# Optimization experiments

Hardware: AMD Instinct MI355X
Metric: run time of the kernel (lower is better)

The kernel has to match this reference:

```python
import jax, jax.numpy as jnp
import numpy as np

DIM = 64        # feature channels of x
HEADS = 4
POS_DIM = 3
NUM_IDS = 8
STR_IN = 512    # strength_linear input size
B, S, W = 4, 1024, 8   # batch, sequence (S1), source-views (S2)


def setup_inputs() -> dict:
    key = jax.random.key(0)
    ks = jax.random.split(key, 18)
    stdv = 1.0 / np.sqrt(DIM * DIM)  # embedding init per module
    d8 = DIM // 8
    u = lambda k, shp, s: jax.random.uniform(k, shp, jnp.float32, -s, s)
    return {
        "x": jax.random.normal(ks[0], (B, DIM, S, W), jnp.float32),
        "pos": jax.random.normal(ks[1], (B, S, POS_DIM), jnp.float32),
        "strength": jax.random.normal(ks[2], (STR_IN,), jnp.float32),
        "embed_id1": 3,
        "q_emb_w": u(ks[3], (NUM_IDS, DIM * DIM), stdv),
        "k_emb_w": u(ks[4], (NUM_IDS, DIM * DIM), stdv),
        "v_emb_w": u(ks[5], (NUM_IDS, DIM * DIM), stdv),
        "pos_w1": u(ks[6], (POS_DIM, POS_DIM), 1.0 / np.sqrt(POS_DIM)),
        "pos_b1": u(ks[7], (POS_DIM,), 1.0 / np.sqrt(POS_DIM)),
        "pos_w2": u(ks[8], (d8, POS_DIM), 1.0 / np.sqrt(POS_DIM)),
        "pos_b2": u(ks[9], (d8,), 1.0 / np.sqrt(POS_DIM)),
        "head_w": u(ks[10], (HEADS, d8), 1.0 / np.sqrt(d8)),
        "head_b": u(ks[11], (HEADS,), 1.0 / np.sqrt(d8)),
        "gate": jnp.ones((HEADS,), jnp.float32),
        "out_w": u(ks[12], (DIM, DIM), 1.0 / np.sqrt(DIM)),
        "out_b": u(ks[13], (DIM,), 1.0 / np.sqrt(DIM)),
        "str_w": u(ks[14], (DIM, STR_IN), 1.0 / np.sqrt(STR_IN)),
        "str_b": u(ks[15], (DIM,), 1.0 / np.sqrt(STR_IN)),
    }


def reference(x, pos, strength, embed_id1, q_emb_w, k_emb_w, v_emb_w,
              pos_w1, pos_b1, pos_w2, pos_b2, head_w, head_b, gate,
              out_w, out_b, str_w, str_b):
    # strength projection: Linear(512, dim)
    s = strength @ str_w.T + str_b                    # [dim]
    xt = jnp.transpose(x, (0, 2, 3, 1))               # [B, S, W, dim]
    qe = q_emb_w[embed_id1].reshape(DIM, DIM)
    ke = k_emb_w[embed_id1].reshape(DIM, DIM)
    ve = v_emb_w[embed_id1].reshape(DIM, DIM)

    def proj(emb):
        y = xt @ emb.T + s                            # [B, S, W, dim]
        # collapse (W, dim) -> (heads, head_dim), heads to axis 1
        y = y.reshape(B, S, HEADS, -1)
        return jnp.transpose(y, (0, 2, 1, 3))         # [B, H, S, hd]

    q, k, v = proj(qe), proj(ke), proj(ve)
    hd = q.shape[-1]
    attn = jax.nn.softmax(jnp.einsum("bhsd,bhtd->bhst", q, k) / np.sqrt(hd), axis=-1)

    # relative-position attention branch
    ph = jax.nn.relu(pos @ pos_w1.T + pos_b1) @ pos_w2.T + pos_b2   # [B, S, dim//8]
    diff = ph[:, :, None, :] - ph[:, None, :, :]                    # [B, S, S, dim//8]
    pos_attn = jnp.transpose(diff @ head_w.T + head_b, (0, 3, 1, 2))
    pos_attn = jax.nn.softmax(pos_attn, axis=-1)                    # [B, H, S, S]

    g = jax.nn.sigmoid(gate).reshape(1, -1, 1, 1)
    attn = (1.0 - g) * attn + g * pos_attn
    attn = attn / jnp.sum(attn, axis=-1, keepdims=True)

    out = jnp.einsum("bhst,bhtd->bhsd", attn, v)      # [B, H, S, hd]
    out = jnp.transpose(out, (0, 2, 1, 3)).reshape(B, S, W, DIM)
    return out @ out_w.T + out_b                      # [B, S, W, dim]
```

## Files before the change

### kernel.cpp

```cpp
#include <hip/hip_runtime.h>
#include <math.h>
#include <stdint.h>

#define B_ 4
#define S_ 1024
#define F_ 512
#define HD 128
#define SOFT_C 4.0f

typedef __attribute__((ext_vector_type(8))) short short8;
typedef __attribute__((ext_vector_type(4))) float f32x4;
typedef __attribute__((ext_vector_type(4))) unsigned int u32x4;
typedef __attribute__((ext_vector_type(2))) unsigned int u32x2;

__device__ __forceinline__ unsigned short f2bf(float f) {
    unsigned int u = __float_as_uint(f);
    u = (u + 0x7FFFu + ((u >> 16) & 1u)) >> 16;
    return (unsigned short)u;
}
__device__ __forceinline__ float bf2f(unsigned int s) {
    return __uint_as_float(s << 16);
}
__device__ __forceinline__ void pack_hilo(const float* v, u32x4& hi, u32x4& lo) {
    #pragma unroll
    for (int p = 0; p < 4; ++p) {
        unsigned int h0 = f2bf(v[2 * p]), h1 = f2bf(v[2 * p + 1]);
        float l0 = v[2 * p] - bf2f(h0), l1 = v[2 * p + 1] - bf2f(h1);
        hi[p] = h0 | (h1 << 16);
        lo[p] = (unsigned int)f2bf(l0) | ((unsigned int)f2bf(l1) << 16);
    }
}

__global__ __launch_bounds__(256) void k_prep(
    const int* __restrict__ embed_id,
    const float* __restrict__ qw, const float* __restrict__ kw,
    const float* __restrict__ vw, const float* __restrict__ ow,
    const float* __restrict__ pos,
    const float* __restrict__ pw1, const float* __restrict__ pb1,
    const float* __restrict__ pw2, const float* __restrict__ pb2,
    const float* __restrict__ head_w,
    const float* __restrict__ strength, const float* __restrict__ str_w,
    const float* __restrict__ str_b,
    unsigned short* __restrict__ packs,
    float* __restrict__ sv, float* __restrict__ svq,
    float* __restrict__ p_g)
{
    __shared__ float red_s[4][4];
    __shared__ float inv_s[4];
    const int blk = blockIdx.x, tid = threadIdx.x;
    const float SCALE = 0.08838834764831845f;

    if (blk < 4) {
        const int id = embed_id[0];
        const float* src = (blk == 0 ? qw + id * 4096 : blk == 1 ? kw + id * 4096
                            : blk == 2 ? vw + id * 4096 : ow);
        const float scale = (blk == 0) ? SCALE : 1.0f;
        unsigned short* hi = packs + blk * 8192;
        unsigned short* lo = hi + 4096;
        for (int i = tid; i < 4096; i += 256) {
            float v = src[i] * scale;
            unsigned short h = f2bf(v);
            hi[i] = h;
            lo[i] = f2bf(v - bf2f(h));
        }
    } else if (blk < 8) {
        const int b = blk - 4;
        const int wv = tid >> 6;
        float w1_[9], b1_[3], w2_[24], b2_[8], hw_[32];
        #pragma unroll
        for (int i = 0; i < 9; ++i)  w1_[i] = pw1[i];
        #pragma unroll
        for (int i = 0; i < 3; ++i)  b1_[i] = pb1[i];
        #pragma unroll
        for (int i = 0; i < 24; ++i) w2_[i] = pw2[i];
        #pragma unroll
        for (int i = 0; i < 8; ++i)  b2_[i] = pb2[i];
        #pragma unroll
        for (int i = 0; i < 32; ++i) hw_[i] = head_w[i];

        float ev[4][4];
        float ps[4] = {0.f, 0.f, 0.f, 0.f};
        #pragma unroll
        for (int k = 0; k < 4; ++k) {
            const int t = k * 256 + tid;
            float p0 = pos[(b * S_ + t) * 3 + 0];
            float p1 = pos[(b * S_ + t) * 3 + 1];
            float p2 = pos[(b * S_ + t) * 3 + 2];
            float h0 = fmaxf(0.f, p0 * w1_[0] + p1 * w1_[1] + p2 * w1_[2] + b1_[0]);
            float h1 = fmaxf(0.f, p0 * w1_[3] + p1 * w1_[4] + p2 * w1_[5] + b1_[1]);
            float h2 = fmaxf(0.f, p0 * w1_[6] + p1 * w1_[7] + p2 * w1_[8] + b1_[2]);
            float ph[8];
            #pragma unroll
            for (int o8 = 0; o8 < 8; ++o8)
                ph[o8] = h0 * w2_[o8 * 3] + h1 * w2_[o8 * 3 + 1] + h2 * w2_[o8 * 3 + 2] + b2_[o8];
            #pragma unroll
            for (int h = 0; h < 4; ++h) {
                float A = 0.f;
                #pragma unroll
                for (int o8 = 0; o8 < 8; ++o8) A += ph[o8] * hw_[h * 8 + o8];
                ev[k][h] = __expf(-A - 1.0f);
                ps[h] += ev[k][h];
            }
        }
        #pragma unroll
        for (int h = 0; h < 4; ++h)
            #pragma unroll
            for (int off = 1; off < 64; off <<= 1)
                ps[h] += __shfl_xor(ps[h], off);
        if ((tid & 63) == 0)
            #pragma unroll
            for (int h = 0; h < 4; ++h) red_s[wv][h] = ps[h];
        __syncthreads();
        if (tid < 4)
            inv_s[tid] = 1.f / (red_s[0][tid] + red_s[1][tid] + red_s[2][tid] + red_s[3][tid]);
        __syncthreads();
        #pragma unroll
        for (int k = 0; k < 4; ++k)
            #pragma unroll
            for (int h = 0; h < 4; ++h)
                p_g[(b * 4 + h) * S_ + k * 256 + tid] = ev[k][h] * inv_s[h];
    } else {
        __shared__ float part_s[4][64];
        const int c = tid & 63, pr = tid >> 6;
        const float* wrow = str_w + c * 512 + pr * 128;
        const float* st   = strength + pr * 128;
        float acc = 0.f;
        #pragma unroll
        for (int j4 = 0; j4 < 32; ++j4) {
            f32x4 wv4 = *(const f32x4*)(wrow + j4 * 4);
            f32x4 s4  = *(const f32x4*)(st + j4 * 4);
            acc += wv4[0] * s4[0] + wv4[1] * s4[1] + wv4[2] * s4[2] + wv4[3] * s4[3];
        }
        part_s[pr][c] = acc;
        __syncthreads();
        if (tid < 64) {
            float v = part_s[0][tid] + part_s[1][tid] + part_s[2][tid]
                    + part_s[3][tid] + str_b[tid];
            sv[tid] = v;
            svq[tid] = v * SCALE;
        }
    }
}

__global__ __launch_bounds__(256) void k_qkv(
    const float* __restrict__ x,
    const unsigned short* __restrict__ packs,
    const float* __restrict__ sv, const float* __restrict__ svq,
    const float* __restrict__ p_g,
    unsigned short* __restrict__ yqh, unsigned short* __restrict__ ykh,
    unsigned short* __restrict__ yvt2, float* __restrict__ xbar)
{
    __shared__ float xr_s[4][8];
    const int tid  = threadIdx.x;
    const int wv   = tid >> 6;
    const int lane = tid & 63;
    const int quad = lane >> 4;
    const int l15  = lane & 15;

    if (blockIdx.x >= 512) {
        const int bi = blockIdx.x - 512;
        const int b = bi >> 6, c = bi & 63;
        const float* xc = x + (size_t)b * 524288 + c * 8192;
        const float* pb = p_g + b * 4096;
        float acc[8] = {};
        #pragma unroll
        for (int rr = 0; rr < 4; ++rr) {
            const int s = tid * 4 + rr;
            f32x4 x0 = *(const f32x4*)(xc + s * 8);
            f32x4 x1 = *(const f32x4*)(xc + s * 8 + 4);
            float p0 = pb[s], p1 = pb[1024 + s], p2 = pb[2048 + s], p3 = pb[3072 + s];
            acc[0] += p0 * x0[0]; acc[1] += p0 * x0[1];
            acc[2] += p1 * x0[2]; acc[3] += p1 * x0[3];
            acc[4] += p2 * x1[0]; acc[5] += p2 * x1[1];
            acc[6] += p3 * x1[2]; acc[7] += p3 * x1[3];
        }
        #pragma unroll
        for (int j = 0; j < 8; ++j)
            #pragma unroll
            for (int off = 1; off < 64; off <<= 1)
                acc[j] += __shfl_xor(acc[j], off);
        if (lane == 0)
            #pragma unroll
            for (int j = 0; j < 8; ++j) xr_s[wv][j] = acc[j];
        __syncthreads();
        if (tid < 8)
            xbar[(b * 8 + tid) * 64 + c] = xr_s[0][tid] + xr_s[1][tid]
                                         + xr_s[2][tid] + xr_s[3][tid];
        return;
    }

    const int r0   = blockIdx.x * 64 + wv * 16;
    const int b    = r0 >> 13;
    const int rloc = (r0 & 8191) + l15;
    const float* xb = x + (size_t)b * 524288;

    u32x4 xhi[2], xlo[2];
    #pragma unroll
    for (int kc = 0; kc < 2; ++kc) {
        float xv[8];
        #pragma unroll
        for (int j = 0; j < 8; ++j)
            xv[j] = xb[(kc * 32 + quad * 8 + j) * 8192 + rloc];
        pack_hilo(xv, xhi[kc], xlo[kc]);
    }

    float svq_l[4], sv_l[4];
    #pragma unroll
    for (int nt = 0; nt < 4; ++nt) {
        svq_l[nt] = svq[nt * 16 + l15];
        sv_l[nt]  = sv[nt * 16 + l15];
    }
    f32x4 svA[4];
    #pragma unroll
    for (int mt = 0; mt < 4; ++mt)
        svA[mt] = *(const f32x4*)(sv + mt * 16 + quad * 4);

    int idxq[4];
    #pragma unroll
    for (int rr = 0; rr < 4; ++rr) {
        const int rl = quad * 4 + rr;
        const int w_ = rl & 7;
        const int s_loc = ((r0 & 8191) >> 3) + (rl >> 3);
        idxq[rr] = (b * 4 + (w_ >> 1)) * 131072 + s_loc * 128 + (w_ & 1) * 64 + l15;
    }

    const int row_g = r0 + l15;
    const int s_idx = (row_g >> 3) & 1023;
    const int w_idx = row_g & 7;
    const int bh    = b * 4 + (w_idx >> 1);
    const int dbase = (w_idx & 1) * 64;
    unsigned short* vtb = yvt2 + (size_t)bh * 131072 + (s_idx >> 6) * 8192
                        + (size_t)dbase * 64 + (s_idx & 63);

    #pragma unroll
    for (int mat = 0; mat < 2; ++mat) {
        const unsigned short* mh = packs + mat * 8192;
        const unsigned short* ml = mh + 4096;
        f32x4 acc[4] = {};
        #pragma unroll
        for (int kc = 0; kc < 2; ++kc)
            #pragma unroll
            for (int nt = 0; nt < 4; ++nt) {
                const int off = (nt * 16 + l15) * 64 + kc * 32 + quad * 8;
                u32x4 ehi = *(const u32x4*)(mh + off);
                u32x4 elo = *(const u32x4*)(ml + off);
                acc[nt] = __builtin_amdgcn_mfma_f32_16x16x32_bf16(
                    __builtin_bit_cast(short8, xhi[kc]),
                    __builtin_bit_cast(short8, ehi), acc[nt], 0, 0, 0);
                acc[nt] = __builtin_amdgcn_mfma_f32_16x16x32_bf16(
                    __builtin_bit_cast(short8, xlo[kc]),
                    __builtin_bit_cast(short8, ehi), acc[nt], 0, 0, 0);
                acc[nt] = __builtin_amdgcn_mfma_f32_16x16x32_bf16(
                    __builtin_bit_cast(short8, xhi[kc]),
                    __builtin_bit_cast(short8, elo), acc[nt], 0, 0, 0);
            }
        unsigned short* y = (mat == 0 ? yqh : ykh);
        const float* svp = (mat == 0 ? svq_l : sv_l);
        #pragma unroll
        for (int nt = 0; nt < 4; ++nt)
            #pragma unroll
            for (int rr = 0; rr < 4; ++rr)
                y[(size_t)idxq[rr] + nt * 16] = f2bf(acc[nt][rr] + svp[nt]);
    }

    {
        const unsigned short* mh = packs + 2 * 8192;
        const unsigned short* ml = mh + 4096;
        f32x4 acc[4] = {};
        #pragma unroll
        for (int kc = 0; kc < 2; ++kc)
            #pragma unroll
            for (int mt = 0; mt < 4; ++mt) {
                const int off = (mt * 16 + l15) * 64 + kc * 32 + quad * 8;
                u32x4 ehi = *(const u32x4*)(mh + off);
                u32x4 elo = *(const u32x4*)(ml + off);
                acc[mt] = __builtin_amdgcn_mfma_f32_16x16x32_bf16(
                    __builtin_bit_cast(short8, ehi),
                    __builtin_bit_cast(short8, xhi[kc]), acc[mt], 0, 0, 0);
                acc[mt] = __builtin_amdgcn_mfma_f32_16x16x32_bf16(
                    __builtin_bit_cast(short8, ehi),
                    __builtin_bit_cast(short8, xlo[kc]), acc[mt], 0, 0, 0);
                acc[mt] = __builtin_amdgcn_mfma_f32_16x16x32_bf16(
                    __builtin_bit_cast(short8, elo),
                    __builtin_bit_cast(short8, xhi[kc]), acc[mt], 0, 0, 0);
            }
        #pragma unroll
        for (int mt = 0; mt < 4; ++mt)
            #pragma unroll
            for (int rr = 0; rr < 4; ++rr) {
                const int c = mt * 16 + quad * 4 + rr;
                vtb[(size_t)c * 64] = f2bf(acc[mt][rr] + svA[mt][rr]);
            }
    }
}

__global__ __launch_bounds__(256, 2) void k_attn(
    const unsigned short* __restrict__ yqh, const unsigned short* __restrict__ ykh,
    const unsigned short* __restrict__ yvt2,
    const float* __restrict__ xbar, const float* __restrict__ vw,
    const int* __restrict__ embed_id, const float* __restrict__ sv,
    const float* __restrict__ gate, float* __restrict__ out)
{
    __shared__ __align__(16) unsigned short kx[2][64 * 136];
    __shared__ __align__(16) unsigned short vx[2][128 * 72];
    __shared__ float vbar_s[128];

    const int tid  = threadIdx.x;
    const int w    = tid >> 6;
    const int lane = tid & 63;
    const int quad = lane >> 4;
    const int l15  = lane & 15;
    const int bh = blockIdx.x & 15, qt = blockIdx.x >> 4;
    const int b = bh >> 2, h = bh & 3;
    const int s0 = qt * 32;
    const int qh = w >> 1;
    const int dh = w & 1;

    const unsigned short* ykb = ykh + (size_t)bh * 131072;
    const unsigned short* yvb = yvt2 + (size_t)bh * 131072;

    if (tid < 128) {
        const int c = tid & 63, wloc = tid >> 6;
        const float* ver = vw + embed_id[0] * 4096 + c * 64;
        const float* xbr = xbar + (b * 8 + h * 2 + wloc) * 64;
        float a = sv[c];
        #pragma unroll
        for (int j4 = 0; j4 < 16; ++j4) {
            f32x4 e4 = *(const f32x4*)(ver + j4 * 4);
            f32x4 x4 = *(const f32x4*)(xbr + j4 * 4);
            a += e4[0] * x4[0] + e4[1] * x4[1] + e4[2] * x4[2] + e4[3] * x4[3];
        }
        vbar_s[wloc * 64 + c] = a;
    }

    u32x4 qf[4];
    #pragma unroll
    for (int kc = 0; kc < 4; ++kc)
        qf[kc] = *(const u32x4*)(yqh + (size_t)bh * 131072
                 + (s0 + qh * 16 + l15) * 128 + kc * 32 + quad * 8);

    #pragma unroll
    for (int r = 0; r < 4; ++r) {
        const int off = r * 2048 + tid * 8;
        *(u32x4*)&kx[0][(off >> 7) * 136 + (off & 127)] =
            *(const u32x4*)(ykb + off);
        *(u32x4*)&vx[0][(off >> 6) * 72 + (off & 63)] =
            *(const u32x4*)(yvb + off);
    }
    __syncthreads();

    f32x4 o[4] = {};
    float lsum = 0.f;
    const int srcA = ((quad & 1) << 5) + l15;

    for (int it = 0; it < 16; ++it) {
        const int cur = it & 1;
        u32x4 kst[4], vst[4];
        const bool pre = (it < 15);
        if (pre) {
            const unsigned short* ksrc = ykb + (it + 1) * 8192;
            const unsigned short* vsrc = yvb + (it + 1) * 8192;
            #pragma unroll
            for (int r = 0; r < 4; ++r)
                kst[r] = *(const u32x4*)(ksrc + r * 2048 + tid * 8);
            #pragma unroll
            for (int r = 0; r < 4; ++r)
                vst[r] = *(const u32x4*)(vsrc + r * 2048 + tid * 8);
        }

        const unsigned short* kxc = kx[cur];
        const unsigned short* vxc = vx[cur];

        #pragma unroll
        for (int th = 0; th < 2; ++th) {
            f32x4 sa0 = {}, sa1 = {};
            #pragma unroll
            for (int kc = 0; kc < 4; ++kc) {
                u32x4 a0 = *(const u32x4*)&kxc[(th * 32 + l15) * 136 + kc * 32 + quad * 8];
                sa0 = __builtin_amdgcn_mfma_f32_16x16x32_bf16(
                    __builtin_bit_cast(short8, a0),
                    __builtin_bit_cast(short8, qf[kc]), sa0, 0, 0, 0);
            }
            #pragma unroll
            for (int kc = 0; kc < 4; ++kc) {
                u32x4 a1 = *(const u32x4*)&kxc[(th * 32 + 16 + l15) * 136 + kc * 32 + quad * 8];
                sa1 = __builtin_amdgcn_mfma_f32_16x16x32_bf16(
                    __builtin_bit_cast(short8, a1),
                    __builtin_bit_cast(short8, qf[kc]), sa1, 0, 0, 0);
            }

            float p0[4], p1[4];
            #pragma unroll
            for (int r = 0; r < 4; ++r) {
                p0[r] = __expf(sa0[r] - SOFT_C);
                p1[r] = __expf(sa1[r] - SOFT_C);
                lsum += p0[r] + p1[r];
            }

            unsigned int pk00 = (unsigned int)f2bf(p0[0]) | ((unsigned int)f2bf(p0[1]) << 16);
            unsigned int pk01 = (unsigned int)f2bf(p0[2]) | ((unsigned int)f2bf(p0[3]) << 16);
            unsigned int pk10 = (unsigned int)f2bf(p1[0]) | ((unsigned int)f2bf(p1[1]) << 16);
            unsigned int pk11 = (unsigned int)f2bf(p1[2]) | ((unsigned int)f2bf(p1[3]) << 16);
            unsigned int sel0 = (quad < 2) ? pk00 : pk10;
            unsigned int sel1 = (quad < 2) ? pk01 : pk11;
            u32x4 pf;
            pf[0] = (unsigned int)__shfl((int)sel0, srcA);
            pf[1] = (unsigned int)__shfl((int)sel1, srcA);
            pf[2] = (unsigned int)__shfl((int)sel0, srcA + 16);
            pf[3] = (unsigned int)__shfl((int)sel1, srcA + 16);

            #pragma unroll
            for (int dt = 0; dt < 4; ++dt) {
                u32x4 vf = *(const u32x4*)&vxc[(dh * 64 + dt * 16 + l15) * 72
                                               + th * 32 + quad * 8];
                o[dt] = __builtin_amdgcn_mfma_f32_16x16x32_bf16(
                    __builtin_bit_cast(short8, vf),
                    __builtin_bit_cast(short8, pf), o[dt], 0, 0, 0);
            }
        }

        if (pre) {
            #pragma unroll
            for (int r = 0; r < 4; ++r) {
                const int off = r * 2048 + tid * 8;
                *(u32x4*)&kx[cur ^ 1][(off >> 7) * 136 + (off & 127)] = kst[r];
            }
            #pragma unroll
            for (int r = 0; r < 4; ++r) {
                const int off = r * 2048 + tid * 8;
                *(u32x4*)&vx[cur ^ 1][(off >> 6) * 72 + (off & 63)] = vst[r];
            }
        }
        __syncthreads();
    }

    lsum += __shfl_xor(lsum, 16);
    lsum += __shfl_xor(lsum, 32);
    const float gf = 1.f / (1.f + __expf(-gate[h]));
    const float cf = (1.f - gf) / lsum;
    const int row = b * S_ + s0 + qh * 16 + l15;
    #pragma unroll
    for (int dt = 0; dt < 4; ++dt) {
        const int d0 = dh * 64 + dt * 16 + quad * 4;
        f32x4 vb = *(const f32x4*)&vbar_s[d0];
        f32x4 rv;
        #pragma unroll
        for (int j = 0; j < 4; ++j) rv[j] = cf * o[dt][j] + gf * vb[j];
        *(f32x4*)(out + (size_t)row * F_ + h * HD + d0) = rv;
    }
}

__global__ __launch_bounds__(256) void k_oproj(
    float* __restrict__ out, const unsigned short* __restrict__ packs,
    const float* __restrict__ ob)
{
    const int tid  = threadIdx.x;
    const int wv   = tid >> 6;
    const int lane = tid & 63;
    const int quad = lane >> 4;
    const int l15  = lane & 15;
    const int r0   = blockIdx.x * 64 + wv * 16;
    const unsigned short* owh = packs + 3 * 8192;
    const unsigned short* owl = owh + 4096;

    u32x4 bhi[2], blo[2];
    #pragma unroll
    for (int kc = 0; kc < 2; ++kc) {
        const float* src = out + (size_t)(r0 + l15) * 64 + kc * 32 + quad * 8;
        f32x4 y0 = *(const f32x4*)src;
        f32x4 y1 = *(const f32x4*)(src + 4);
        float yv8[8] = {y0[0], y0[1], y0[2], y0[3], y1[0], y1[1], y1[2], y1[3]};
        pack_hilo(yv8, bhi[kc], blo[kc]);
    }

    f32x4 acc[4] = {};
    #pragma unroll
    for (int kc = 0; kc < 2; ++kc)
        #pragma unroll
        for (int mt = 0; mt < 4; ++mt) {
            const int off = (mt * 16 + l15) * 64 + kc * 32 + quad * 8;
            u32x4 ahi = *(const u32x4*)(owh + off);
            u32x4 alo = *(const u32x4*)(owl + off);
            acc[mt] = __builtin_amdgcn_mfma_f32_16x16x32_bf16(
                __builtin_bit_cast(short8, ahi),
                __builtin_bit_cast(short8, bhi[kc]), acc[mt], 0, 0, 0);
            acc[mt] = __builtin_amdgcn_mfma_f32_16x16x32_bf16(
                __builtin_bit_cast(short8, ahi),
                __builtin_bit_cast(short8, blo[kc]), acc[mt], 0, 0, 0);
            acc[mt] = __builtin_amdgcn_mfma_f32_16x16x32_bf16(
                __builtin_bit_cast(short8, alo),
                __builtin_bit_cast(short8, bhi[kc]), acc[mt], 0, 0, 0);
        }

    #pragma unroll
    for (int mt = 0; mt < 4; ++mt) {
        f32x4 bias = *(const f32x4*)(ob + mt * 16 + quad * 4);
        f32x4 v = acc[mt] + bias;
        *(f32x4*)(out + (size_t)(r0 + l15) * 64 + mt * 16 + quad * 4) = v;
    }
}

extern "C" void kernel_launch(void* const* d_in, const int* in_sizes, int n_in,
                              void* d_out, int out_size, void* d_ws, size_t ws_size,
                              hipStream_t stream) {
    (void)in_sizes; (void)n_in; (void)out_size; (void)ws_size;
    const float* x        = (const float*)d_in[0];
    const float* pos      = (const float*)d_in[1];
    const float* strength = (const float*)d_in[2];
    const int*   embed_id = (const int*)d_in[3];
    const float* qw       = (const float*)d_in[4];
    const float* kw       = (const float*)d_in[5];
    const float* vw       = (const float*)d_in[6];
    const float* pw1      = (const float*)d_in[7];
    const float* pb1      = (const float*)d_in[8];
    const float* pw2      = (const float*)d_in[9];
    const float* pb2      = (const float*)d_in[10];
    const float* head_w   = (const float*)d_in[11];
    const float* gate     = (const float*)d_in[13];
    const float* out_w    = (const float*)d_in[14];
    const float* out_b    = (const float*)d_in[15];
    const float* str_w    = (const float*)d_in[16];
    const float* str_b    = (const float*)d_in[17];
    float* out = (float*)d_out;

    unsigned short* yqh   = (unsigned short*)d_ws;
    unsigned short* ykh   = yqh + 2097152;
    unsigned short* yvt2  = ykh + 2097152;
    unsigned short* packs = yvt2 + 2097152;
    float* sv   = (float*)(packs + 8 * 4096);
    float* svq  = sv + 64;
    float* p_g  = svq + 64;
    float* xbar = p_g + 16384;

    k_prep<<<9, 256, 0, stream>>>(embed_id, qw, kw, vw, out_w, pos,
                                  pw1, pb1, pw2, pb2, head_w,
                                  strength, str_w, str_b, packs, sv, svq, p_g);
    k_qkv<<<768, 256, 0, stream>>>(x, packs, sv, svq, p_g, yqh, ykh, yvt2, xbar);
    k_attn<<<512, 256, 0, stream>>>(yqh, ykh, yvt2, xbar, vw, embed_id, sv,
                                    gate, out);
    k_oproj<<<512, 256, 0, stream>>>(out, packs, out_b);
}
```

Before: 157.1 us.

## Fuse prep into QKV kernel and output projection into attention kernel

Removes the separate prep and output-projection launches. Each QKV block now computes the strength projection itself and packs the embedding weights into hi/lo bf16 on the fly, and the xbar blocks compute the position softmax locally. The attention kernel applies out_w to its tile through LDS-staged hi/lo MFMAs and folds the gated vbar term through the projection, avoiding a round trip of the attention output through global memory. The cost is redundant per-block work (strength GEMV, weight packing, position MLP) and extra LDS and register pressure.

```diff
diff --git a/kernel.cpp b/kernel.cpp
--- a/kernel.cpp
+++ b/kernel.cpp
@@ -31,41 +31,37 @@
     }
 }
 
-__global__ __launch_bounds__(256) void k_prep(
+__global__ __launch_bounds__(256) void k_qkv(
+    const float* __restrict__ x, const float* __restrict__ strength,
     const int* __restrict__ embed_id,
     const float* __restrict__ qw, const float* __restrict__ kw,
-    const float* __restrict__ vw, const float* __restrict__ ow,
+    const float* __restrict__ vw,
+    const float* __restrict__ str_w, const float* __restrict__ str_b,
     const float* __restrict__ pos,
     const float* __restrict__ pw1, const float* __restrict__ pb1,
     const float* __restrict__ pw2, const float* __restrict__ pb2,
     const float* __restrict__ head_w,
-    const float* __restrict__ strength, const float* __restrict__ str_w,
-    const float* __restrict__ str_b,
-    unsigned short* __restrict__ packs,
-    float* __restrict__ sv, float* __restrict__ svq,
-    float* __restrict__ p_g)
+    unsigned short* __restrict__ yqh, unsigned short* __restrict__ ykh,
+    unsigned short* __restrict__ yvt2,
+    float* __restrict__ xbar, float* __restrict__ sv_g)
 {
+    __shared__ float p_s[4096];
+    __shared__ float part_s[4][64];
+    __shared__ float sv_s[64], svq_s[64];
     __shared__ float red_s[4][4];
     __shared__ float inv_s[4];
-    const int blk = blockIdx.x, tid = threadIdx.x;
+    __shared__ float xr_s[4][8];
+
+    const int tid  = threadIdx.x;
+    const int wv   = tid >> 6;
+    const int lane = tid & 63;
+    const int quad = lane >> 4;
+    const int l15  = lane & 15;
     const float SCALE = 0.08838834764831845f;
 
-    if (blk < 4) {
-        const int id = embed_id[0];
-        const float* src = (blk == 0 ? qw + id * 4096 : blk == 1 ? kw + id * 4096
-                            : blk == 2 ? vw + id * 4096 : ow);
-        const float scale = (blk == 0) ? SCALE : 1.0f;
-        unsigned short* hi = packs + blk * 8192;
-        unsigned short* lo = hi + 4096;
-        for (int i = tid; i < 4096; i += 256) {
-            float v = src[i] * scale;
-            unsigned short h = f2bf(v);
-            hi[i] = h;
-            lo[i] = f2bf(v - bf2f(h));
-        }
-    } else if (blk < 8) {
-        const int b = blk - 4;
-        const int wv = tid >> 6;
+    if (blockIdx.x >= 512) {
+        const int bi = blockIdx.x - 512;
+        const int b = bi >> 6, c = bi & 63;
         float w1_[9], b1_[3], w2_[24], b2_[8], hw_[32];
         #pragma unroll
         for (int i = 0; i < 9; ++i)  w1_[i] = pw1[i];
@@ -78,7 +74,6 @@
         #pragma unroll
         for (int i = 0; i < 32; ++i) hw_[i] = head_w[i];
 
-        float ev[4][4];
         float ps[4] = {0.f, 0.f, 0.f, 0.f};
         #pragma unroll
         for (int k = 0; k < 4; ++k) {
@@ -98,8 +93,9 @@
                 float A = 0.f;
                 #pragma unroll
                 for (int o8 = 0; o8 < 8; ++o8) A += ph[o8] * hw_[h * 8 + o8];
-                ev[k][h] = __expf(-A - 1.0f);
-                ps[h] += ev[k][h];
+                float e = __expf(-A - 1.0f);
+                p_s[h * 1024 + t] = e;
+                ps[h] += e;
             }
         }
         #pragma unroll
@@ -107,23 +103,45 @@
             #pragma unroll
             for (int off = 1; off < 64; off <<= 1)
                 ps[h] += __shfl_xor(ps[h], off);
-        if ((tid & 63) == 0)
+        if (lane == 0)
             #pragma unroll
             for (int h = 0; h < 4; ++h) red_s[wv][h] = ps[h];
         __syncthreads();
         if (tid < 4)
             inv_s[tid] = 1.f / (red_s[0][tid] + red_s[1][tid] + red_s[2][tid] + red_s[3][tid]);
         __syncthreads();
-        #pragma unroll
-        for (int k = 0; k < 4; ++k)
-            #pragma unroll
-            for (int h = 0; h < 4; ++h)
-                p_g[(b * 4 + h) * S_ + k * 256 + tid] = ev[k][h] * inv_s[h];
-    } else {
-        __shared__ float part_s[4][64];
-        const int c = tid & 63, pr = tid >> 6;
-        const float* wrow = str_w + c * 512 + pr * 128;
-        const float* st   = strength + pr * 128;
+
+        const float* xc = x + (size_t)b * 524288 + c * 8192;
+        float acc[8] = {};
+        #pragma unroll
+        for (int rr = 0; rr < 4; ++rr) {
+            const int s = tid * 4 + rr;
+            f32x4 x0 = *(const f32x4*)(xc + s * 8);
+            f32x4 x1 = *(const f32x4*)(xc + s * 8 + 4);
+            float p0 = p_s[s], p1 = p_s[1024 + s], p2 = p_s[2048 + s], p3 = p_s[3072 + s];
+            acc[0] += p0 * x0[0]; acc[1] += p0 * x0[1];
+            acc[2] += p1 * x0[2]; acc[3] += p1 * x0[3];
+            acc[4] += p2 * x1[0]; acc[5] += p2 * x1[1];
+            acc[6] += p3 * x1[2]; acc[7] += p3 * x1[3];
+        }
+        #pragma unroll
+        for (int j = 0; j < 8; ++j)
+            #pragma unroll
+            for (int off = 1; off < 64; off <<= 1)
+                acc[j] += __shfl_xor(acc[j], off);
+        if (lane == 0)
+            #pragma unroll
+            for (int j = 0; j < 8; ++j) xr_s[wv][j] = acc[j];
+        __syncthreads();
+        if (tid < 8)
+            xbar[(b * 8 + tid) * 64 + c] = (xr_s[0][tid] + xr_s[1][tid]
+                + xr_s[2][tid] + xr_s[3][tid]) * inv_s[tid >> 1];
+        return;
+    }
+
+    {
+        const float* wrow = str_w + lane * 512 + wv * 128;
+        const float* st   = strength + wv * 128;
         float acc = 0.f;
         #pragma unroll
         for (int j4 = 0; j4 < 32; ++j4) {
@@ -131,68 +149,23 @@
             f32x4 s4  = *(const f32x4*)(st + j4 * 4);
             acc += wv4[0] * s4[0] + wv4[1] * s4[1] + wv4[2] * s4[2] + wv4[3] * s4[3];
         }
-        part_s[pr][c] = acc;
-        __syncthreads();
-        if (tid < 64) {
-            float v = part_s[0][tid] + part_s[1][tid] + part_s[2][tid]
-                    + part_s[3][tid] + str_b[tid];
-            sv[tid] = v;
-            svq[tid] = v * SCALE;
-        }
-    }
-}
-
-__global__ __launch_bounds__(256) void k_qkv(
-    const float* __restrict__ x,
-    const unsigned short* __restrict__ packs,
-    const float* __restrict__ sv, const float* __restrict__ svq,
-    const float* __restrict__ p_g,
-    unsigned short* __restrict__ yqh, unsigned short* __restrict__ ykh,
-    unsigned short* __restrict__ yvt2, float* __restrict__ xbar)
-{
-    __shared__ float xr_s[4][8];
-    const int tid  = threadIdx.x;
-    const int wv   = tid >> 6;
-    const int lane = tid & 63;
-    const int quad = lane >> 4;
-    const int l15  = lane & 15;
-
-    if (blockIdx.x >= 512) {
-        const int bi = blockIdx.x - 512;
-        const int b = bi >> 6, c = bi & 63;
-        const float* xc = x + (size_t)b * 524288 + c * 8192;
-        const float* pb = p_g + b * 4096;
-        float acc[8] = {};
-        #pragma unroll
-        for (int rr = 0; rr < 4; ++rr) {
-            const int s = tid * 4 + rr;
-            f32x4 x0 = *(const f32x4*)(xc + s * 8);
-            f32x4 x1 = *(const f32x4*)(xc + s * 8 + 4);
-            float p0 = pb[s], p1 = pb[1024 + s], p2 = pb[2048 + s], p3 = pb[3072 + s];
-            acc[0] += p0 * x0[0]; acc[1] += p0 * x0[1];
-            acc[2] += p1 * x0[2]; acc[3] += p1 * x0[3];
-            acc[4] += p2 * x1[0]; acc[5] += p2 * x1[1];
-            acc[6] += p3 * x1[2]; acc[7] += p3 * x1[3];
-        }
-        #pragma unroll
-        for (int j = 0; j < 8; ++j)
-            #pragma unroll
-            for (int off = 1; off < 64; off <<= 1)
-                acc[j] += __shfl_xor(acc[j], off);
-        if (lane == 0)
-            #pragma unroll
-            for (int j = 0; j < 8; ++j) xr_s[wv][j] = acc[j];
-        __syncthreads();
-        if (tid < 8)
-            xbar[(b * 8 + tid) * 64 + c] = xr_s[0][tid] + xr_s[1][tid]
-                                         + xr_s[2][tid] + xr_s[3][tid];
-        return;
-    }
+        part_s[wv][lane] = acc;
+    }
+    __syncthreads();
+    if (wv == 0) {
+        float v = part_s[0][lane] + part_s[1][lane] + part_s[2][lane]
+                + part_s[3][lane] + str_b[lane];
+        sv_s[lane] = v;
+        svq_s[lane] = v * SCALE;
+    }
+    __syncthreads();
+    if (blockIdx.x == 0 && tid < 64) sv_g[tid] = sv_s[tid];
 
     const int r0   = blockIdx.x * 64 + wv * 16;
     const int b    = r0 >> 13;
     const int rloc = (r0 & 8191) + l15;
     const float* xb = x + (size_t)b * 524288;
+    const int id = embed_id[0];
 
     u32x4 xhi[2], xlo[2];
     #pragma unroll
@@ -207,13 +180,13 @@
     float svq_l[4], sv_l[4];
     #pragma unroll
     for (int nt = 0; nt < 4; ++nt) {
-        svq_l[nt] = svq[nt * 16 + l15];
-        sv_l[nt]  = sv[nt * 16 + l15];
+        svq_l[nt] = svq_s[nt * 16 + l15];
+        sv_l[nt]  = sv_s[nt * 16 + l15];
     }
     f32x4 svA[4];
     #pragma unroll
     for (int mt = 0; mt < 4; ++mt)
-        svA[mt] = *(const f32x4*)(sv + mt * 16 + quad * 4);
+        svA[mt] = *(const f32x4*)(&sv_s[mt * 16 + quad * 4]);
 
     int idxq[4];
     #pragma unroll
@@ -223,7 +196,6 @@
         const int s_loc = ((r0 & 8191) >> 3) + (rl >> 3);
         idxq[rr] = (b * 4 + (w_ >> 1)) * 131072 + s_loc * 128 + (w_ & 1) * 64 + l15;
     }
-
     const int row_g = r0 + l15;
     const int s_idx = (row_g >> 3) & 1023;
     const int w_idx = row_g & 7;
@@ -232,65 +204,68 @@
     unsigned short* vtb = yvt2 + (size_t)bh * 131072 + (s_idx >> 6) * 8192
                         + (size_t)dbase * 64 + (s_idx & 63);
 
-    #pragma unroll
-    for (int mat = 0; mat < 2; ++mat) {
-        const unsigned short* mh = packs + mat * 8192;
-        const unsigned short* ml = mh + 4096;
+    for (int mat = 0; mat < 3; ++mat) {
+        const float* em = (mat == 0 ? qw : mat == 1 ? kw : vw) + id * 4096;
+        const float msc = (mat == 0) ? SCALE : 1.0f;
+        u32x4 ehi[4][2], elo[4][2];
+        #pragma unroll
+        for (int nt = 0; nt < 4; ++nt)
+            #pragma unroll
+            for (int kc = 0; kc < 2; ++kc) {
+                const float* src = em + (nt * 16 + l15) * 64 + kc * 32 + quad * 8;
+                f32x4 e0 = *(const f32x4*)src;
+                f32x4 e1 = *(const f32x4*)(src + 4);
+                float ev[8] = {e0[0] * msc, e0[1] * msc, e0[2] * msc, e0[3] * msc,
+                               e1[0] * msc, e1[1] * msc, e1[2] * msc, e1[3] * msc};
+                pack_hilo(ev, ehi[nt][kc], elo[nt][kc]);
+            }
+
         f32x4 acc[4] = {};
-        #pragma unroll
-        for (int kc = 0; kc < 2; ++kc)
-            #pragma unroll
-            for (int nt = 0; nt < 4; ++nt) {
-                const int off = (nt * 16 + l15) * 64 + kc * 32 + quad * 8;
-                u32x4 ehi = *(const u32x4*)(mh + off);
-                u32x4 elo = *(const u32x4*)(ml + off);
-                acc[nt] = __builtin_amdgcn_mfma_f32_16x16x32_bf16(
-                    __builtin_bit_cast(short8, xhi[kc]),
-                    __builtin_bit_cast(short8, ehi), acc[nt], 0, 0, 0);
-                acc[nt] = __builtin_amdgcn_mfma_f32_16x16x32_bf16(
-                    __builtin_bit_cast(short8, xlo[kc]),
-                    __builtin_bit_cast(short8, ehi), acc[nt], 0, 0, 0);
-                acc[nt] = __builtin_amdgcn_mfma_f32_16x16x32_bf16(
-                    __builtin_bit_cast(short8, xhi[kc]),
-                    __builtin_bit_cast(short8, elo), acc[nt], 0, 0, 0);
-            }
-        unsigned short* y = (mat == 0 ? yqh : ykh);
-        const float* svp = (mat == 0 ? svq_l : sv_l);
-        #pragma unroll
-        for (int nt = 0; nt < 4; ++nt)
-            #pragma unroll
-            for (int rr = 0; rr < 4; ++rr)
-                y[(size_t)idxq[rr] + nt * 16] = f2bf(acc[nt][rr] + svp[nt]);
-    }
-
-    {
-        const unsigned short* mh = packs + 2 * 8192;
-        const unsigned short* ml = mh + 4096;
-        f32x4 acc[4] = {};
-        #pragma unroll
-        for (int kc = 0; kc < 2; ++kc)
-            #pragma unroll
-            for (int mt = 0; mt < 4; ++mt) {
-                const int off = (mt * 16 + l15) * 64 + kc * 32 + quad * 8;
-                u32x4 ehi = *(const u32x4*)(mh + off);
-                u32x4 elo = *(const u32x4*)(ml + off);
-                acc[mt] = __builtin_amdgcn_mfma_f32_16x16x32_bf16(
-                    __builtin_bit_cast(short8, ehi),
-                    __builtin_bit_cast(short8, xhi[kc]), acc[mt], 0, 0, 0);
-                acc[mt] = __builtin_amdgcn_mfma_f32_16x16x32_bf16(
-                    __builtin_bit_cast(short8, ehi),
-                    __builtin_bit_cast(short8, xlo[kc]), acc[mt], 0, 0, 0);
-                acc[mt] = __builtin_amdgcn_mfma_f32_16x16x32_bf16(
-                    __builtin_bit_cast(short8, elo),
-                    __builtin_bit_cast(short8, xhi[kc]), acc[mt], 0, 0, 0);
-            }
-        #pragma unroll
-        for (int mt = 0; mt < 4; ++mt)
-            #pragma unroll
-            for (int rr = 0; rr < 4; ++rr) {
-                const int c = mt * 16 + quad * 4 + rr;
-                vtb[(size_t)c * 64] = f2bf(acc[mt][rr] + svA[mt][rr]);
-            }
+        if (mat < 2) {
+            #pragma unroll
+            for (int kc = 0; kc < 2; ++kc)
+                #pragma unroll
+                for (int nt = 0; nt < 4; ++nt) {
+                    acc[nt] = __builtin_amdgcn_mfma_f32_16x16x32_bf16(
+                        __builtin_bit_cast(short8, xhi[kc]),
+                        __builtin_bit_cast(short8, ehi[nt][kc]), acc[nt], 0, 0, 0);
+                    acc[nt] = __builtin_amdgcn_mfma_f32_16x16x32_bf16(
+                        __builtin_bit_cast(short8, xlo[kc]),
+                        __builtin_bit_cast(short8, ehi[nt][kc]), acc[nt], 0, 0, 0);
+                    acc[nt] = __builtin_amdgcn_mfma_f32_16x16x32_bf16(
+                        __builtin_bit_cast(short8, xhi[kc]),
+                        __builtin_bit_cast(short8, elo[nt][kc]), acc[nt], 0, 0, 0);
+                }
+            unsigned short* y = (mat == 0 ? yqh : ykh);
+            const float* svp = (mat == 0 ? svq_l : sv_l);
+            #pragma unroll
+            for (int nt = 0; nt < 4; ++nt)
+                #pragma unroll
+                for (int rr = 0; rr < 4; ++rr)
+                    y[(size_t)idxq[rr] + nt * 16] = f2bf(acc[nt][rr] + svp[nt]);
+        } else {
+            #pragma unroll
+            for (int kc = 0; kc < 2; ++kc)
+                #pragma unroll
+                for (int mt = 0; mt < 4; ++mt) {
+                    acc[mt] = __builtin_amdgcn_mfma_f32_16x16x32_bf16(
+                        __builtin_bit_cast(short8, ehi[mt][kc]),
+                        __builtin_bit_cast(short8, xhi[kc]), acc[mt], 0, 0, 0);
+                    acc[mt] = __builtin_amdgcn_mfma_f32_16x16x32_bf16(
+                        __builtin_bit_cast(short8, ehi[mt][kc]),
+                        __builtin_bit_cast(short8, xlo[kc]), acc[mt], 0, 0, 0);
+                    acc[mt] = __builtin_amdgcn_mfma_f32_16x16x32_bf16(
+                        __builtin_bit_cast(short8, elo[mt][kc]),
+                        __builtin_bit_cast(short8, xhi[kc]), acc[mt], 0, 0, 0);
+                }
+            #pragma unroll
+            for (int mt = 0; mt < 4; ++mt)
+                #pragma unroll
+                for (int rr = 0; rr < 4; ++rr) {
+                    const int c = mt * 16 + quad * 4 + rr;
+                    vtb[(size_t)c * 64] = f2bf(acc[mt][rr] + svA[mt][rr]);
+                }
+        }
     }
 }
 
@@ -298,12 +273,15 @@
     const unsigned short* __restrict__ yqh, const unsigned short* __restrict__ ykh,
     const unsigned short* __restrict__ yvt2,
     const float* __restrict__ xbar, const float* __restrict__ vw,
-    const int* __restrict__ embed_id, const float* __restrict__ sv,
-    const float* __restrict__ gate, float* __restrict__ out)
+    const int* __restrict__ embed_id, const float* __restrict__ sv_g,
+    const float* __restrict__ gate,
+    const float* __restrict__ ow, const float* __restrict__ ob,
+    float* __restrict__ out)
 {
     __shared__ __align__(16) unsigned short kx[2][64 * 136];
     __shared__ __align__(16) unsigned short vx[2][128 * 72];
     __shared__ float vbar_s[128];
+    __shared__ float vproj_s[128];
 
     const int tid  = threadIdx.x;
     const int w    = tid >> 6;
@@ -318,12 +296,13 @@
 
     const unsigned short* ykb = ykh + (size_t)bh * 131072;
     const unsigned short* yvb = yvt2 + (size_t)bh * 131072;
+    const float gf = 1.f / (1.f + __expf(-gate[h]));
 
     if (tid < 128) {
         const int c = tid & 63, wloc = tid >> 6;
         const float* ver = vw + embed_id[0] * 4096 + c * 64;
         const float* xbr = xbar + (b * 8 + h * 2 + wloc) * 64;
-        float a = sv[c];
+        float a = sv_g[c];
         #pragma unroll
         for (int j4 = 0; j4 < 16; ++j4) {
             f32x4 e4 = *(const f32x4*)(ver + j4 * 4);
@@ -348,6 +327,20 @@
             *(const u32x4*)(yvb + off);
     }
     __syncthreads();
+
+    if (tid < 128) {
+        const int cp = tid & 63, w2 = tid >> 6;
+        const float* owr = ow + cp * 64;
+        const float* vb = vbar_s + w2 * 64;
+        float a = 0.f;
+        #pragma unroll
+        for (int j4 = 0; j4 < 16; ++j4) {
+            f32x4 o4 = *(const f32x4*)(owr + j4 * 4);
+            f32x4 v4 = *(const f32x4*)(vb + j4 * 4);
+            a += o4[0] * v4[0] + o4[1] * v4[1] + o4[2] * v4[2] + o4[3] * v4[3];
+        }
+        vproj_s[tid] = gf * a + ob[cp];
+    }
 
     f32x4 o[4] = {};
     float lsum = 0.f;
@@ -436,67 +429,63 @@
 
     lsum += __shfl_xor(lsum, 16);
     lsum += __shfl_xor(lsum, 32);
-    const float gf = 1.f / (1.f + __expf(-gate[h]));
     const float cf = (1.f - gf) / lsum;
-    const int row = b * S_ + s0 + qh * 16 + l15;
+
+    unsigned short* yst = (unsigned short*)kx + w * 4352;
     #pragma unroll
     for (int dt = 0; dt < 4; ++dt) {
-        const int d0 = dh * 64 + dt * 16 + quad * 4;
-        f32x4 vb = *(const f32x4*)&vbar_s[d0];
-        f32x4 rv;
-        #pragma unroll
-        for (int j = 0; j < 4; ++j) rv[j] = cf * o[dt][j] + gf * vb[j];
-        *(f32x4*)(out + (size_t)row * F_ + h * HD + d0) = rv;
-    }
-}
-
-__global__ __launch_bounds__(256) void k_oproj(
-    float* __restrict__ out, const unsigned short* __restrict__ packs,
-    const float* __restrict__ ob)
-{
-    const int tid  = threadIdx.x;
-    const int wv   = tid >> 6;
-    const int lane = tid & 63;
-    const int quad = lane >> 4;
-    const int l15  = lane & 15;
-    const int r0   = blockIdx.x * 64 + wv * 16;
-    const unsigned short* owh = packs + 3 * 8192;
-    const unsigned short* owl = owh + 4096;
-
-    u32x4 bhi[2], blo[2];
+        f32x4 yv = o[dt];
+        unsigned int hh[4];
+        unsigned short ll[4];
+        #pragma unroll
+        for (int r = 0; r < 4; ++r) {
+            float y = cf * yv[r];
+            hh[r] = f2bf(y);
+            ll[r] = f2bf(y - bf2f(hh[r]));
+        }
+        const int dloc = dt * 16 + quad * 4;
+        u32x2 ph_, pl_;
+        ph_[0] = hh[0] | (hh[1] << 16);
+        ph_[1] = hh[2] | (hh[3] << 16);
+        pl_[0] = (unsigned int)ll[0] | ((unsigned int)ll[1] << 16);
+        pl_[1] = (unsigned int)ll[2] | ((unsigned int)ll[3] << 16);
+        *(u32x2*)&yst[l15 * 68 + dloc] = ph_;
+        *(u32x2*)&yst[1088 + l15 * 68 + dloc] = pl_;
+    }
+    u32x4 ybh[2], ybl[2];
     #pragma unroll
     for (int kc = 0; kc < 2; ++kc) {
-        const float* src = out + (size_t)(r0 + l15) * 64 + kc * 32 + quad * 8;
-        f32x4 y0 = *(const f32x4*)src;
-        f32x4 y1 = *(const f32x4*)(src + 4);
-        float yv8[8] = {y0[0], y0[1], y0[2], y0[3], y1[0], y1[1], y1[2], y1[3]};
-        pack_hilo(yv8, bhi[kc], blo[kc]);
-    }
-
-    f32x4 acc[4] = {};
+        ybh[kc] = *(const u32x4*)&yst[l15 * 68 + kc * 32 + quad * 8];
+        ybl[kc] = *(const u32x4*)&yst[1088 + l15 * 68 + kc * 32 + quad * 8];
+    }
+    f32x4 accp[4] = {};
     #pragma unroll
     for (int kc = 0; kc < 2; ++kc)
         #pragma unroll
         for (int mt = 0; mt < 4; ++mt) {
-            const int off = (mt * 16 + l15) * 64 + kc * 32 + quad * 8;
-            u32x4 ahi = *(const u32x4*)(owh + off);
-            u32x4 alo = *(const u32x4*)(owl + off);
-            acc[mt] = __builtin_amdgcn_mfma_f32_16x16x32_bf16(
-                __builtin_bit_cast(short8, ahi),
-                __builtin_bit_cast(short8, bhi[kc]), acc[mt], 0, 0, 0);
-            acc[mt] = __builtin_amdgcn_mfma_f32_16x16x32_bf16(
-                __builtin_bit_cast(short8, ahi),
-                __builtin_bit_cast(short8, blo[kc]), acc[mt], 0, 0, 0);
-            acc[mt] = __builtin_amdgcn_mfma_f32_16x16x32_bf16(
-                __builtin_bit_cast(short8, alo),
-                __builtin_bit_cast(short8, bhi[kc]), acc[mt], 0, 0, 0);
-        }
-
+            const float* src = ow + (mt * 16 + l15) * 64 + kc * 32 + quad * 8;
+            f32x4 e0 = *(const f32x4*)src;
+            f32x4 e1 = *(const f32x4*)(src + 4);
+            float ev[8] = {e0[0], e0[1], e0[2], e0[3], e1[0], e1[1], e1[2], e1[3]};
+            u32x4 ohi, olo;
+            pack_hilo(ev, ohi, olo);
+            accp[mt] = __builtin_amdgcn_mfma_f32_16x16x32_bf16(
+                __builtin_bit_cast(short8, ohi),
+                __builtin_bit_cast(short8, ybh[kc]), accp[mt], 0, 0, 0);
+            accp[mt] = __builtin_amdgcn_mfma_f32_16x16x32_bf16(
+                __builtin_bit_cast(short8, ohi),
+                __builtin_bit_cast(short8, ybl[kc]), accp[mt], 0, 0, 0);
+            accp[mt] = __builtin_amdgcn_mfma_f32_16x16x32_bf16(
+                __builtin_bit_cast(short8, olo),
+                __builtin_bit_cast(short8, ybh[kc]), accp[mt], 0, 0, 0);
+        }
+    const int sQ = s0 + qh * 16 + l15;
+    float* op = out + ((size_t)((b * S_ + sQ) * 8 + 2 * h + dh)) * 64;
     #pragma unroll
     for (int mt = 0; mt < 4; ++mt) {
-        f32x4 bias = *(const f32x4*)(ob + mt * 16 + quad * 4);
-        f32x4 v = acc[mt] + bias;
-        *(f32x4*)(out + (size_t)(r0 + l15) * 64 + mt * 16 + quad * 4) = v;
+        f32x4 vp = *(const f32x4*)&vproj_s[dh * 64 + mt * 16 + quad * 4];
+        f32x4 rv = accp[mt] + vp;
+        *(f32x4*)(op + mt * 16 + quad * 4) = rv;
     }
 }
 
@@ -523,20 +512,15 @@
     const float* str_b    = (const float*)d_in[17];
     float* out = (float*)d_out;
 
-    unsigned short* yqh   = (unsigned short*)d_ws;
-    unsigned short* ykh   = yqh + 2097152;
-    unsigned short* yvt2  = ykh + 2097152;
-    unsigned short* packs = yvt2 + 2097152;
-    float* sv   = (float*)(packs + 8 * 4096);
-    float* svq  = sv + 64;
-    float* p_g  = svq + 64;
-    float* xbar = p_g + 16384;
-
-    k_prep<<<9, 256, 0, stream>>>(embed_id, qw, kw, vw, out_w, pos,
-                                  pw1, pb1, pw2, pb2, head_w,
-                                  strength, str_w, str_b, packs, sv, svq, p_g);
-    k_qkv<<<768, 256, 0, stream>>>(x, packs, sv, svq, p_g, yqh, ykh, yvt2, xbar);
-    k_attn<<<512, 256, 0, stream>>>(yqh, ykh, yvt2, xbar, vw, embed_id, sv,
-                                    gate, out);
-    k_oproj<<<512, 256, 0, stream>>>(out, packs, out_b);
+    unsigned short* yqh  = (unsigned short*)d_ws;
+    unsigned short* ykh  = yqh + 2097152;
+    unsigned short* yvt2 = ykh + 2097152;
+    float* xbar = (float*)(yvt2 + 2097152);
+    float* sv_g = xbar + 2048;
+
+    k_qkv<<<768, 256, 0, stream>>>(x, strength, embed_id, qw, kw, vw,
+                                   str_w, str_b, pos, pw1, pb1, pw2, pb2,
+                                   head_w, yqh, ykh, yvt2, xbar, sv_g);
+    k_attn<<<512, 256, 0, stream>>>(yqh, ykh, yvt2, xbar, vw, embed_id, sv_g,
+                                    gate, out_w, out_b, out);
 }
```

After: 157.9 us. Within noise of the previous version (+0.5%).
